# Kernel tuning notes

Measured on AMD Instinct MI355X. Metric: run time of the kernel, lower is better.

The kernel has to match this reference:

```python
import jax, jax.numpy as jnp
import numpy as np

EPS = 1e-5
OFFSET_SCALE = 1.0
KPTS = 9   # 3x3 deformable kernel
GROUP = 1  # in_dim // out_dim


def _bn(x, g, b, m, v):
    # eval-mode BatchNorm2d on (B,C,H,W)
    s = g / jnp.sqrt(v + EPS)
    return x * s[None, :, None, None] + (b - m * s)[None, :, None, None]


def _dcnv4_core(value, offset, mask, offset_scale):
    # value: (B,H,W,G,Cg); offset: (B,H,W,G,K,2) as (dx,dy); mask: (B,H,W,G,K)
    B, H, W, G, Cg = value.shape
    K = mask.shape[-1]
    dt = value.dtype
    ky = jnp.repeat(jnp.arange(3) - 1, 3).astype(dt)
    kx = jnp.tile(jnp.arange(3) - 1, 3).astype(dt)
    grid = jnp.stack([kx, ky], -1)                                   # (K,2)
    base = jnp.stack(jnp.meshgrid(jnp.arange(W, dtype=dt),
                                  jnp.arange(H, dtype=dt),
                                  indexing='xy'), -1)                # (H,W,2) = (x,y)
    loc = base[None, :, :, None, None, :] + (grid + offset) * offset_scale  # (B,H,W,G,K,2)
    px, py = loc[..., 0], loc[..., 1]
    x0 = jnp.floor(px); y0 = jnp.floor(py)
    fx = px - x0; fy = py - y0
    vflat = value.transpose(0, 3, 1, 2, 4).reshape(B, G, H * W, Cg)
    out = jnp.zeros((B, G, H * W, Cg), dt)
    corners = ((0.0, 0.0, (1 - fx) * (1 - fy)), (1.0, 0.0, fx * (1 - fy)),
               (0.0, 1.0, (1 - fx) * fy), (1.0, 1.0, fx * fy))
    for dx, dy, wgt in corners:
        xi = x0 + dx; yi = y0 + dy
        valid = ((xi >= 0) & (xi < W) & (yi >= 0) & (yi < H)).astype(dt)
        idx = (jnp.clip(yi, 0, W and H - 1) * W + jnp.clip(xi, 0, W - 1)).astype(jnp.int32)
        idx = idx.transpose(0, 3, 1, 2, 4).reshape(B, G, H * W * K)
        v = jnp.take_along_axis(vflat, idx[..., None], axis=2).reshape(B, G, H * W, K, Cg)
        w = (wgt * valid * mask).transpose(0, 3, 1, 2, 4).reshape(B, G, H * W, K)
        out = out + jnp.einsum('bgsk,bgskc->bgsc', w, v)
    return out.reshape(B, G, H, W, Cg).transpose(0, 2, 3, 1, 4).reshape(B, H, W, G * Cg)


def setup_inputs() -> dict:
    key = jax.random.key(0)
    B, C, H, W = 8, 128, 64, 64
    C_OUT = 128
    OM = ((GROUP * KPTS * 3 + 7) // 8) * 8  # 32, offset_mask padded width
    ks = jax.random.split(key, 16)
    f = jnp.float32
    sc = 1.0 / np.sqrt(C).astype(np.float32)
    return {
        'x': jax.random.normal(ks[0], (B, C, H, W), f),
        'bn1_g': jax.random.uniform(ks[1], (C,), f, 0.5, 1.5),
        'bn1_b': jax.random.normal(ks[2], (C,), f) * 0.1,
        'bn1_m': jax.random.normal(ks[3], (C,), f) * 0.1,
        'bn1_v': jax.random.uniform(ks[4], (C,), f, 0.5, 1.5),
        'w_pw0': jax.random.normal(ks[5], (C, C), f) * sc,
        'w_vp': jax.random.normal(ks[6], (C, C), f) * sc,
        'b_vp': jnp.zeros((C,), f),
        'w_om': jax.random.normal(ks[7], (C, OM), f) * 0.01,
        'b_om': jnp.zeros((OM,), f),
        'w_op': jax.random.normal(ks[8], (C, C), f) * sc,
        'bn2_g': jax.random.uniform(ks[9], (C,), f, 0.5, 1.5),
        'bn2_b': jax.random.normal(ks[10], (C,), f) * 0.1,
        'bn2_m': jax.random.normal(ks[11], (C,), f) * 0.1,
        'bn2_v': jax.random.uniform(ks[12], (C,), f, 0.5, 1.5),
        'w_pw1': jax.random.normal(ks[13], (C_OUT, C), f) * sc,
    }


def reference(x, bn1_g, bn1_b, bn1_m, bn1_v, w_pw0, w_vp, b_vp, w_om, b_om, w_op,
              bn2_g, bn2_b, bn2_m, bn2_v, w_pw1):
    x = _bn(x, bn1_g, bn1_b, bn1_m, bn1_v)
    x = jnp.einsum('bchw,oc->bohw', x, w_pw0)
    B, C, H, W = x.shape
    x = x.reshape(B, H * W, C)  # raw reshape (faithful to torch .reshape, NOT a permute)
    G, K = GROUP, KPTS
    Cg = C // G
    value = (x @ w_vp + b_vp).reshape(B, H, W, G, Cg)
    om = (x @ w_om + b_om)[..., :G * K * 3].reshape(B, H, W, G, K, 3)
    out = _dcnv4_core(value, om[..., :2], om[..., 2], OFFSET_SCALE)
    out = out.reshape(B, H * W, C) @ w_op
    x = out.reshape(B, C, H, W)  # raw reshape back
    x = _bn(x, bn2_g, bn2_b, bn2_m, bn2_v)
    x = jnp.einsum('bchw,oc->bohw', x, w_pw1)
    return x
```

## Files before the change

### kernel.cpp

```cpp
#include <hip/hip_runtime.h>

#define HW 4096
typedef unsigned short ushort;
typedef __attribute__((ext_vector_type(8))) short short8;
typedef __attribute__((ext_vector_type(4))) float f32x4;

__device__ __forceinline__ ushort bf_rne(float f) {
  unsigned u = __float_as_uint(f);
  unsigned r = (u + 0x7fffu + ((u >> 16) & 1u)) >> 16;
  return (ushort)r;
}
__device__ __forceinline__ void split2(float f, ushort& hi, ushort& lo) {
  ushort h = bf_rne(f);
  float hf = __uint_as_float((unsigned)h << 16);
  hi = h;
  lo = bf_rne(f - hf);
}

__global__ __launch_bounds__(256) void prep(
    const float* __restrict__ g1, const float* __restrict__ be1,
    const float* __restrict__ m1, const float* __restrict__ v1,
    const float* __restrict__ w0,
    const float* __restrict__ g2, const float* __restrict__ be2,
    const float* __restrict__ m2, const float* __restrict__ v2,
    const float* __restrict__ w1,
    const float* __restrict__ wvp, const float* __restrict__ wom,
    const float* __restrict__ wop,
    ushort* __restrict__ W0h, ushort* __restrict__ W0l, float* __restrict__ b0,
    ushort* __restrict__ W1h, ushort* __restrict__ W1l, float* __restrict__ b1,
    ushort* __restrict__ vph, ushort* __restrict__ vpl,
    ushort* __restrict__ oph, ushort* __restrict__ opl,
    ushort* __restrict__ omh, ushort* __restrict__ oml)
{
  const int t = threadIdx.x;
  const int role = blockIdx.x;
  if (role < 16) {
    __shared__ float sc[128], sh[128], part[16][17];
    const int cv = role >> 3;
    const float* g  = cv ? g2 : g1;
    const float* be = cv ? be2 : be1;
    const float* mm = cv ? m2 : m1;
    const float* vv = cv ? v2 : v1;
    if (t < 128) {
      float s = g[t] / sqrtf(vv[t] + 1e-5f);
      sc[t] = s;
      sh[t] = be[t] - mm[t] * s;
    }
    __syncthreads();
    const float* ws = cv ? w1 : w0;
    ushort* dh = cv ? W1h : W0h;
    ushort* dl = cv ? W1l : W0l;
    float* bb  = cv ? b1 : b0;
    const int o = ((role & 7) << 4) + (t >> 4);
    const int kl = t & 15;
    float accb = 0.f;
    #pragma unroll
    for (int j = 0; j < 8; ++j) {
      const int k = (kl << 3) + j;
      const float wv = ws[o * 128 + k];
      ushort hi, lo;
      split2(wv * sc[k], hi, lo);
      dh[o * 128 + k] = hi;
      dl[o * 128 + k] = lo;
      accb = fmaf(wv, sh[k], accb);
    }
    part[t >> 4][kl] = accb;
    __syncthreads();
    if (kl == 0) {
      float s = 0.f;
      #pragma unroll
      for (int j = 0; j < 16; ++j) s += part[t >> 4][j];
      bb[o] = s;
    }
  } else if (role < 32) {
    const int rr = role & 7;
    const float* srcM = (role < 24) ? wvp : wop;
    ushort* dh = (role < 24) ? vph : oph;
    ushort* dl = (role < 24) ? vpl : opl;
    const int n = (rr << 4) + (t >> 4);
    const int kl = t & 15;
    #pragma unroll
    for (int j = 0; j < 8; ++j) {
      const int k = (kl << 3) + j;
      ushort hi, lo;
      split2(srcM[k * 128 + n], hi, lo);
      dh[n * 128 + k] = hi;
      dl[n * 128 + k] = lo;
    }
  } else {
    const int n = ((role - 32) << 4) + (t >> 4);
    const int kl = t & 15;
    #pragma unroll
    for (int j = 0; j < 8; ++j) {
      const int k = (kl << 3) + j;
      ushort hi, lo;
      split2(wom[k * 32 + n], hi, lo);
      omh[n * 128 + k] = hi;
      oml[n * 128 + k] = lo;
    }
  }
}

__global__ __launch_bounds__(256) void gemm_wx(
    const float* __restrict__ act, const ushort* __restrict__ Wh,
    const ushort* __restrict__ Wl, const float* __restrict__ bias,
    float* __restrict__ out)
{
  __shared__ __align__(16) ushort Ah[128][32], Al[128][32];
  __shared__ __align__(16) ushort Bh[128][32], Bl[128][32];
  __shared__ float bias_s[128];
  const int t = threadIdx.x;
  const int hwBase = blockIdx.x << 7;
  const size_t base = (size_t)blockIdx.y * (size_t)(128 * HW);
  if (t < 128) bias_s[t] = bias[t];
  const int lane = t & 63, w = t >> 6;
  const int col = lane & 15, quad = lane >> 4;
  const int wm = (w & 1) << 6, wn = (w >> 1) << 6;
  const f32x4 z = {0.f, 0.f, 0.f, 0.f};
  f32x4 acc[4][4];
  #pragma unroll
  for (int i = 0; i < 4; ++i)
    #pragma unroll
    for (int j = 0; j < 4; ++j) acc[i][j] = z;

  for (int kc = 0; kc < 4; ++kc) {
    const int kBase = kc << 5;
    #pragma unroll
    for (int i = 0; i < 2; ++i) {
      const int idx = t + (i << 8);
      const int o = idx >> 2, q = (idx & 3) << 3;
      *(uint4*)&Ah[o][q] = *(const uint4*)&Wh[o * 128 + kBase + q];
      *(uint4*)&Al[o][q] = *(const uint4*)&Wl[o * 128 + kBase + q];
    }
    {
      const int kr = t >> 3, j0 = (t & 7) << 4;
      const float* srow = &act[base + (size_t)(kBase + kr) * HW + hwBase + j0];
      #pragma unroll
      for (int c4 = 0; c4 < 4; ++c4) {
        const float4 f = *(const float4*)(srow + (c4 << 2));
        ushort h0, l0, h1, l1, h2, l2, h3, l3;
        split2(f.x, h0, l0); split2(f.y, h1, l1);
        split2(f.z, h2, l2); split2(f.w, h3, l3);
        const int j = j0 + (c4 << 2);
        Bh[j + 0][kr] = h0; Bl[j + 0][kr] = l0;
        Bh[j + 1][kr] = h1; Bl[j + 1][kr] = l1;
        Bh[j + 2][kr] = h2; Bl[j + 2][kr] = l2;
        Bh[j + 3][kr] = h3; Bl[j + 3][kr] = l3;
      }
    }
    __syncthreads();
    short8 ah[4], al[4], bh[4], bl[4];
    #pragma unroll
    for (int f = 0; f < 4; ++f) {
      const int row = wm + (f << 4) + col;
      ah[f] = *(const short8*)&Ah[row][quad << 3];
      al[f] = *(const short8*)&Al[row][quad << 3];
    }
    #pragma unroll
    for (int g = 0; g < 4; ++g) {
      const int row = wn + (g << 4) + col;
      bh[g] = *(const short8*)&Bh[row][quad << 3];
      bl[g] = *(const short8*)&Bl[row][quad << 3];
    }
    #pragma unroll
    for (int f = 0; f < 4; ++f)
      #pragma unroll
      for (int g = 0; g < 4; ++g) {
        acc[f][g] = __builtin_amdgcn_mfma_f32_16x16x32_bf16(ah[f], bh[g], acc[f][g], 0, 0, 0);
        acc[f][g] = __builtin_amdgcn_mfma_f32_16x16x32_bf16(ah[f], bl[g], acc[f][g], 0, 0, 0);
        acc[f][g] = __builtin_amdgcn_mfma_f32_16x16x32_bf16(al[f], bh[g], acc[f][g], 0, 0, 0);
      }
    __syncthreads();
  }
  #pragma unroll
  for (int f = 0; f < 4; ++f)
    #pragma unroll
    for (int r = 0; r < 4; ++r) {
      const int o = wm + (f << 4) + (quad << 2) + r;
      const float bb = bias_s[o];
      #pragma unroll
      for (int g = 0; g < 4; ++g)
        out[base + (size_t)o * HW + hwBase + wn + (g << 4) + col] = acc[f][g][r] + bb;
    }
}

template<int NF, bool VALOM>
__global__ __launch_bounds__(256) void gemm_an(
    const float* __restrict__ src,
    const ushort* __restrict__ BTh, const ushort* __restrict__ BTl,
    const ushort* __restrict__ BT2h, const ushort* __restrict__ BT2l,
    const float* __restrict__ bias1, const float* __restrict__ bias2,
    float* __restrict__ C1, float* __restrict__ C2)
{
  __shared__ __align__(16) ushort Ah[128][32], Al[128][32];
  __shared__ __align__(16) ushort Bh[NF * 32][32], Bl[NF * 32][32];
  const int t = threadIdx.x;
  const int rBase = blockIdx.x << 7;
  const int lane = t & 63, w = t >> 6;
  const int col = lane & 15, quad = lane >> 4;
  const int wm = (w & 1) << 6;
  const int wn = (w >> 1) * (NF * 16);
  const f32x4 z = {0.f, 0.f, 0.f, 0.f};
  f32x4 acc[4][NF];
  #pragma unroll
  for (int i = 0; i < 4; ++i)
    #pragma unroll
    for (int j = 0; j < NF; ++j) acc[i][j] = z;

  for (int kc = 0; kc < 4; ++kc) {
    const int kBase = kc << 5;
    {
      const int row = t >> 1, kh = (t & 1) << 4;
      const float* sr = &src[(size_t)(rBase + row) * 128 + kBase + kh];
      union { ushort u[8]; uint4 v; } ph, pl;
      #pragma unroll
      for (int half = 0; half < 2; ++half) {
        #pragma unroll
        for (int c4 = 0; c4 < 2; ++c4) {
          const float4 f = *(const float4*)(sr + (half << 3) + (c4 << 2));
          split2(f.x, ph.u[c4 * 4 + 0], pl.u[c4 * 4 + 0]);
          split2(f.y, ph.u[c4 * 4 + 1], pl.u[c4 * 4 + 1]);
          split2(f.z, ph.u[c4 * 4 + 2], pl.u[c4 * 4 + 2]);
          split2(f.w, ph.u[c4 * 4 + 3], pl.u[c4 * 4 + 3]);
        }
        *(uint4*)&Ah[row][kh + (half << 3)] = ph.v;
        *(uint4*)&Al[row][kh + (half << 3)] = pl.v;
      }
    }
    for (int i = t; i < NF * 32 * 4; i += 256) {
      const int n = i >> 2, q = (i & 3) << 3;
      const ushort* ph = (VALOM && n >= 128) ? &BT2h[(n - 128) * 128 + kBase + q]
                                             : &BTh[n * 128 + kBase + q];
      const ushort* pl = (VALOM && n >= 128) ? &BT2l[(n - 128) * 128 + kBase + q]
                                             : &BTl[n * 128 + kBase + q];
      *(uint4*)&Bh[n][q] = *(const uint4*)ph;
      *(uint4*)&Bl[n][q] = *(const uint4*)pl;
    }
    __syncthreads();
    short8 ah[4], al[4];
    #pragma unroll
    for (int f = 0; f < 4; ++f) {
      const int row = wm + (f << 4) + col;
      ah[f] = *(const short8*)&Ah[row][quad << 3];
      al[f] = *(const short8*)&Al[row][quad << 3];
    }
    #pragma unroll
    for (int g = 0; g < NF; ++g) {
      const int row = wn + (g << 4) + col;
      const short8 bh = *(const short8*)&Bh[row][quad << 3];
      const short8 bl = *(const short8*)&Bl[row][quad << 3];
      #pragma unroll
      for (int f = 0; f < 4; ++f) {
        acc[f][g] = __builtin_amdgcn_mfma_f32_16x16x32_bf16(ah[f], bh, acc[f][g], 0, 0, 0);
        acc[f][g] = __builtin_amdgcn_mfma_f32_16x16x32_bf16(ah[f], bl, acc[f][g], 0, 0, 0);
        acc[f][g] = __builtin_amdgcn_mfma_f32_16x16x32_bf16(al[f], bh, acc[f][g], 0, 0, 0);
      }
    }
    __syncthreads();
  }
  int ng[NF];
  float bb[NF];
  #pragma unroll
  for (int g = 0; g < NF; ++g) {
    ng[g] = wn + (g << 4) + col;
    bb[g] = VALOM ? (ng[g] < 128 ? bias1[ng[g]] : bias2[ng[g] - 128]) : 0.f;
  }
  #pragma unroll
  for (int f = 0; f < 4; ++f)
    #pragma unroll
    for (int r = 0; r < 4; ++r) {
      const int m = rBase + wm + (f << 4) + (quad << 2) + r;
      #pragma unroll
      for (int g = 0; g < NF; ++g) {
        const float v = acc[f][g][r] + bb[g];
        if (VALOM) {
          if (ng[g] < 128) C1[(size_t)m * 128 + ng[g]] = v;
          else             C2[(size_t)m * 32 + (ng[g] - 128)] = v;
        } else {
          C1[(size_t)m * 128 + ng[g]] = v;
        }
      }
    }
}

__global__ __launch_bounds__(256) void dcn_sample(
    const float* __restrict__ value, const float* __restrict__ om,
    float* __restrict__ out)
{
  __shared__ float oms[8][32];
  const int t = threadIdx.x;
  const int blk = blockIdx.x;
  const int b = blk >> 9;
  const int sBase = (blk & 511) << 3;
  const int s = sBase + (t >> 5);
  const int cg = (t & 31) << 2;
  oms[t >> 5][t & 31] = om[((size_t)b * HW + sBase + (t >> 5)) * 32 + (t & 31)];
  __syncthreads();
  const int h = s >> 6, wq = s & 63;
  const float* vb = value + (size_t)b * HW * 128;
  const float* omp = oms[t >> 5];
  const float fw = (float)wq, fh = (float)h;
  float4 acc = {0.f, 0.f, 0.f, 0.f};
  #pragma unroll
  for (int k = 0; k < 9; ++k) {
    const float kx = (float)(k % 3 - 1);
    const float ky = (float)(k / 3 - 1);
    const float dx = omp[k * 3 + 0];
    const float dy = omp[k * 3 + 1];
    const float m  = omp[k * 3 + 2];
    const float px = fw + kx + dx;
    const float py = fh + ky + dy;
    const float x0f = floorf(px), y0f = floorf(py);
    const float fx = px - x0f, fy = py - y0f;
    const int ix = (int)x0f, iy = (int)y0f;
    #pragma unroll
    for (int cy = 0; cy < 2; ++cy) {
      const int yi = iy + cy;
      const float wy = cy ? fy : 1.f - fy;
      const float vy = (yi >= 0 && yi < 64) ? 1.f : 0.f;
      const int yc = min(max(yi, 0), 63);
      #pragma unroll
      for (int cx = 0; cx < 2; ++cx) {
        const int xi = ix + cx;
        const float wx = cx ? fx : 1.f - fx;
        const float vx = (xi >= 0 && xi < 64) ? 1.f : 0.f;
        const int xc = min(max(xi, 0), 63);
        const float wgt = wx * wy * vx * vy * m;
        const float4 v = *(const float4*)&vb[(size_t)(yc * 64 + xc) * 128 + cg];
        acc.x = fmaf(wgt, v.x, acc.x);
        acc.y = fmaf(wgt, v.y, acc.y);
        acc.z = fmaf(wgt, v.z, acc.z);
        acc.w = fmaf(wgt, v.w, acc.w);
      }
    }
  }
  *(float4*)&out[((size_t)b * HW + s) * 128 + cg] = acc;
}

extern "C" void kernel_launch(void* const* d_in, const int* in_sizes, int n_in,
                              void* d_out, int out_size, void* d_ws, size_t ws_size,
                              hipStream_t stream)
{
  const float* x    = (const float*)d_in[0];
  const float* g1   = (const float*)d_in[1];
  const float* be1  = (const float*)d_in[2];
  const float* m1   = (const float*)d_in[3];
  const float* v1   = (const float*)d_in[4];
  const float* wpw0 = (const float*)d_in[5];
  const float* wvp  = (const float*)d_in[6];
  const float* bvp  = (const float*)d_in[7];
  const float* womW = (const float*)d_in[8];
  const float* bom  = (const float*)d_in[9];
  const float* wop  = (const float*)d_in[10];
  const float* g2   = (const float*)d_in[11];
  const float* be2  = (const float*)d_in[12];
  const float* m2   = (const float*)d_in[13];
  const float* v2   = (const float*)d_in[14];
  const float* wpw1 = (const float*)d_in[15];

  char* ws = (char*)d_ws;
  float* y2    = (float*)(ws + 0);
  float* samp  = (float*)(ws + 0);
  float* value = (float*)(ws + 16777216);
  float* out2  = (float*)(ws + 16777216);
  float* omb   = (float*)(ws + 33554432);
  size_t o = 37748736;
  ushort* W0h = (ushort*)(ws + o); o += 32768;
  ushort* W0l = (ushort*)(ws + o); o += 32768;
  ushort* W1h = (ushort*)(ws + o); o += 32768;
  ushort* W1l = (ushort*)(ws + o); o += 32768;
  ushort* vph = (ushort*)(ws + o); o += 32768;
  ushort* vpl = (ushort*)(ws + o); o += 32768;
  ushort* oph = (ushort*)(ws + o); o += 32768;
  ushort* opl = (ushort*)(ws + o); o += 32768;
  ushort* omh = (ushort*)(ws + o); o += 8192;
  ushort* oml = (ushort*)(ws + o); o += 8192;
  float*  b0  = (float*)(ws + o);  o += 512;
  float*  b1  = (float*)(ws + o);

  prep<<<34, 256, 0, stream>>>(g1, be1, m1, v1, wpw0, g2, be2, m2, v2, wpw1,
                               wvp, womW, wop,
                               W0h, W0l, b0, W1h, W1l, b1,
                               vph, vpl, oph, opl, omh, oml);
  gemm_wx<<<dim3(32, 8), 256, 0, stream>>>(x, W0h, W0l, b0, y2);
  gemm_an<5, true><<<dim3(256), 256, 0, stream>>>(y2, vph, vpl, omh, oml,
                                                  bvp, bom, value, omb);
  dcn_sample<<<dim3(4096), 256, 0, stream>>>(value, omb, samp);
  gemm_an<4, false><<<dim3(256), 256, 0, stream>>>(samp, oph, opl, nullptr, nullptr,
                                                   nullptr, nullptr, out2, nullptr);
  gemm_wx<<<dim3(32, 8), 256, 0, stream>>>(out2, W1h, W1l, b1, (float*)d_out);
}
```

Before: 169.8 us.

## Fuse back-to-back GEMM pairs and emit split-bf16 samples from sampler

Fuses the pointwise conv GEMM with the value/offset-mask projection GEMM in one kernel, and the output projection with the final pointwise conv in another. The intermediate stays in shared memory, and the raw-reshape index mapping is used to pick which rows each block owns. The sampler now writes hi/lo bf16 halves directly, so the later GEMM skips the fp32 load and split. This cuts two kernel launches and about two full fp32 intermediate round-trips through HBM. In exchange, only 256 blocks run each fused GEMM, and the kernels use more registers and shared memory, which may limit occupancy.

```diff
diff --git a/kernel.cpp b/kernel.cpp
--- a/kernel.cpp
+++ b/kernel.cpp
@@ -1,6 +1,7 @@
 #include <hip/hip_runtime.h>
 
 #define HW 4096
+#define PAD 33
 typedef unsigned short ushort;
 typedef __attribute__((ext_vector_type(8))) short short8;
 typedef __attribute__((ext_vector_type(4))) float f32x4;
@@ -101,191 +102,150 @@
   }
 }
 
-__global__ __launch_bounds__(256) void gemm_wx(
-    const float* __restrict__ act, const ushort* __restrict__ Wh,
-    const ushort* __restrict__ Wl, const float* __restrict__ bias,
-    float* __restrict__ out)
+__global__ __launch_bounds__(256) void fused_x_valom(
+    const float* __restrict__ x,
+    const ushort* __restrict__ W0h, const ushort* __restrict__ W0l,
+    const float* __restrict__ b0,
+    const ushort* __restrict__ vph, const ushort* __restrict__ vpl,
+    const float* __restrict__ bvp, const float* __restrict__ bom,
+    float* __restrict__ value, float* __restrict__ omb)
 {
-  __shared__ __align__(16) ushort Ah[128][32], Al[128][32];
-  __shared__ __align__(16) ushort Bh[128][32], Bl[128][32];
-  __shared__ float bias_s[128];
+  __shared__ __align__(16) char smem[37376];
+  __shared__ float b0_s[128], b2_s[160];
+  ushort (*Wh_s)[32] = (ushort(*)[32])(smem);
+  ushort (*Wl_s)[32] = (ushort(*)[32])(smem + 8192);
+  float*  Xf         = (float*)(smem + 16384);
+  float*  Yf         = (float*)(smem);
+  ushort (*Vh_s)[32] = (ushort(*)[32])(smem + 16896);
+  ushort (*Vl_s)[32] = (ushort(*)[32])(smem + 27136);
+
   const int t = threadIdx.x;
-  const int hwBase = blockIdx.x << 7;
-  const size_t base = (size_t)blockIdx.y * (size_t)(128 * HW);
-  if (t < 128) bias_s[t] = bias[t];
+  const int cb = blockIdx.x;
+  const int b = blockIdx.y;
+  const int hwBase = cb << 7;
+  const size_t xbase = (size_t)b * (size_t)(128 * HW);
+  if (t < 128) b0_s[t] = b0[t];
+  if (t < 160) b2_s[t] = (t < 128) ? bvp[t] : bom[t - 128];
   const int lane = t & 63, w = t >> 6;
   const int col = lane & 15, quad = lane >> 4;
-  const int wm = (w & 1) << 6, wn = (w >> 1) << 6;
+  const int wm1 = (w & 1) << 6, wn1 = (w >> 1) << 6;
   const f32x4 z = {0.f, 0.f, 0.f, 0.f};
-  f32x4 acc[4][4];
+
+  f32x4 acc1[4][4];
   #pragma unroll
   for (int i = 0; i < 4; ++i)
     #pragma unroll
-    for (int j = 0; j < 4; ++j) acc[i][j] = z;
+    for (int j = 0; j < 4; ++j) acc1[i][j] = z;
 
   for (int kc = 0; kc < 4; ++kc) {
-    const int kBase = kc << 5;
-    #pragma unroll
-    for (int i = 0; i < 2; ++i) {
-      const int idx = t + (i << 8);
-      const int o = idx >> 2, q = (idx & 3) << 3;
-      *(uint4*)&Ah[o][q] = *(const uint4*)&Wh[o * 128 + kBase + q];
-      *(uint4*)&Al[o][q] = *(const uint4*)&Wl[o * 128 + kBase + q];
-    }
-    {
-      const int kr = t >> 3, j0 = (t & 7) << 4;
-      const float* srow = &act[base + (size_t)(kBase + kr) * HW + hwBase + j0];
-      #pragma unroll
-      for (int c4 = 0; c4 < 4; ++c4) {
-        const float4 f = *(const float4*)(srow + (c4 << 2));
-        ushort h0, l0, h1, l1, h2, l2, h3, l3;
-        split2(f.x, h0, l0); split2(f.y, h1, l1);
-        split2(f.z, h2, l2); split2(f.w, h3, l3);
-        const int j = j0 + (c4 << 2);
-        Bh[j + 0][kr] = h0; Bl[j + 0][kr] = l0;
-        Bh[j + 1][kr] = h1; Bl[j + 1][kr] = l1;
-        Bh[j + 2][kr] = h2; Bl[j + 2][kr] = l2;
-        Bh[j + 3][kr] = h3; Bl[j + 3][kr] = l3;
-      }
-    }
-    __syncthreads();
-    short8 ah[4], al[4], bh[4], bl[4];
+    const int kB = kc << 5;
+    for (int i = t; i < 512; i += 256) {
+      const int o = i >> 2, q8 = (i & 3) << 3;
+      *(uint4*)&Wh_s[o][q8] = *(const uint4*)&W0h[o * 128 + kB + q8];
+      *(uint4*)&Wl_s[o][q8] = *(const uint4*)&W0l[o * 128 + kB + q8];
+    }
+    #pragma unroll
+    for (int p = 0; p < 4; ++p) {
+      const int idx = (p << 8) + t;
+      const int c = idx >> 5, j4 = (idx & 31) << 2;
+      const float4 f = *(const float4*)&x[xbase + (size_t)(kB + c) * HW + hwBase + j4];
+      Xf[(j4 + 0) * PAD + c] = f.x;
+      Xf[(j4 + 1) * PAD + c] = f.y;
+      Xf[(j4 + 2) * PAD + c] = f.z;
+      Xf[(j4 + 3) * PAD + c] = f.w;
+    }
+    __syncthreads();
+    short8 aH[4], aL[4];
     #pragma unroll
     for (int f = 0; f < 4; ++f) {
-      const int row = wm + (f << 4) + col;
-      ah[f] = *(const short8*)&Ah[row][quad << 3];
-      al[f] = *(const short8*)&Al[row][quad << 3];
+      const int row = wm1 + (f << 4) + col;
+      aH[f] = *(const short8*)&Wh_s[row][quad << 3];
+      aL[f] = *(const short8*)&Wl_s[row][quad << 3];
     }
     #pragma unroll
     for (int g = 0; g < 4; ++g) {
-      const int row = wn + (g << 4) + col;
-      bh[g] = *(const short8*)&Bh[row][quad << 3];
-      bl[g] = *(const short8*)&Bl[row][quad << 3];
-    }
-    #pragma unroll
-    for (int f = 0; f < 4; ++f)
-      #pragma unroll
-      for (int g = 0; g < 4; ++g) {
-        acc[f][g] = __builtin_amdgcn_mfma_f32_16x16x32_bf16(ah[f], bh[g], acc[f][g], 0, 0, 0);
-        acc[f][g] = __builtin_amdgcn_mfma_f32_16x16x32_bf16(ah[f], bl[g], acc[f][g], 0, 0, 0);
-        acc[f][g] = __builtin_amdgcn_mfma_f32_16x16x32_bf16(al[f], bh[g], acc[f][g], 0, 0, 0);
-      }
-    __syncthreads();
-  }
-  #pragma unroll
-  for (int f = 0; f < 4; ++f)
+      const float* xr = &Xf[(wn1 + (g << 4) + col) * PAD + (quad << 3)];
+      union { ushort u[8]; short8 v; } bh, bl;
+      #pragma unroll
+      for (int j = 0; j < 8; ++j) split2(xr[j], bh.u[j], bl.u[j]);
+      #pragma unroll
+      for (int f = 0; f < 4; ++f) {
+        acc1[f][g] = __builtin_amdgcn_mfma_f32_16x16x32_bf16(aH[f], bh.v, acc1[f][g], 0, 0, 0);
+        acc1[f][g] = __builtin_amdgcn_mfma_f32_16x16x32_bf16(aH[f], bl.v, acc1[f][g], 0, 0, 0);
+        acc1[f][g] = __builtin_amdgcn_mfma_f32_16x16x32_bf16(aL[f], bh.v, acc1[f][g], 0, 0, 0);
+      }
+    }
+    __syncthreads();
+  }
+
+  const int wm2 = (w & 1) << 6;
+  const int wn2 = (w >> 1) * 80;
+  f32x4 acc2[4][5];
+  #pragma unroll
+  for (int i = 0; i < 4; ++i)
+    #pragma unroll
+    for (int j = 0; j < 5; ++j) acc2[i][j] = z;
+
+  for (int j2 = 0; j2 < 4; ++j2) {
+    for (int i = t; i < 640; i += 256) {
+      const int n = i >> 2, q8 = (i & 3) << 3;
+      *(uint4*)&Vh_s[n][q8] = *(const uint4*)&vph[n * 128 + (j2 << 5) + q8];
+      *(uint4*)&Vl_s[n][q8] = *(const uint4*)&vpl[n * 128 + (j2 << 5) + q8];
+    }
+    if ((w >> 1) == (j2 >> 1)) {
+      #pragma unroll
+      for (int gg = 0; gg < 2; ++gg) {
+        const int g = ((j2 & 1) << 1) + gg;
+        #pragma unroll
+        for (int f = 0; f < 4; ++f) {
+          const int o = wm1 + (f << 4) + (quad << 2);
+          #pragma unroll
+          for (int r = 0; r < 4; ++r)
+            Yf[(o + r) * PAD + (gg << 4) + col] = acc1[f][g][r] + b0_s[o + r];
+        }
+      }
+    }
+    __syncthreads();
+    union { ushort u[8]; short8 v; } a2h[4], a2l[4];
+    #pragma unroll
+    for (int f2 = 0; f2 < 4; ++f2) {
+      const float* yr = &Yf[(wm2 + (f2 << 4) + col) * PAD + (quad << 3)];
+      #pragma unroll
+      for (int j = 0; j < 8; ++j) split2(yr[j], a2h[f2].u[j], a2l[f2].u[j]);
+    }
+    #pragma unroll
+    for (int g2 = 0; g2 < 5; ++g2) {
+      const int n = wn2 + (g2 << 4) + col;
+      const short8 vh = *(const short8*)&Vh_s[n][quad << 3];
+      const short8 vl = *(const short8*)&Vl_s[n][quad << 3];
+      #pragma unroll
+      for (int f2 = 0; f2 < 4; ++f2) {
+        acc2[f2][g2] = __builtin_amdgcn_mfma_f32_16x16x32_bf16(a2h[f2].v, vh, acc2[f2][g2], 0, 0, 0);
+        acc2[f2][g2] = __builtin_amdgcn_mfma_f32_16x16x32_bf16(a2h[f2].v, vl, acc2[f2][g2], 0, 0, 0);
+        acc2[f2][g2] = __builtin_amdgcn_mfma_f32_16x16x32_bf16(a2l[f2].v, vh, acc2[f2][g2], 0, 0, 0);
+      }
+    }
+    __syncthreads();
+  }
+  #pragma unroll
+  for (int f2 = 0; f2 < 4; ++f2)
     #pragma unroll
     for (int r = 0; r < 4; ++r) {
-      const int o = wm + (f << 4) + (quad << 2) + r;
-      const float bb = bias_s[o];
-      #pragma unroll
-      for (int g = 0; g < 4; ++g)
-        out[base + (size_t)o * HW + hwBase + wn + (g << 4) + col] = acc[f][g][r] + bb;
-    }
-}
-
-template<int NF, bool VALOM>
-__global__ __launch_bounds__(256) void gemm_an(
-    const float* __restrict__ src,
-    const ushort* __restrict__ BTh, const ushort* __restrict__ BTl,
-    const ushort* __restrict__ BT2h, const ushort* __restrict__ BT2l,
-    const float* __restrict__ bias1, const float* __restrict__ bias2,
-    float* __restrict__ C1, float* __restrict__ C2)
-{
-  __shared__ __align__(16) ushort Ah[128][32], Al[128][32];
-  __shared__ __align__(16) ushort Bh[NF * 32][32], Bl[NF * 32][32];
-  const int t = threadIdx.x;
-  const int rBase = blockIdx.x << 7;
-  const int lane = t & 63, w = t >> 6;
-  const int col = lane & 15, quad = lane >> 4;
-  const int wm = (w & 1) << 6;
-  const int wn = (w >> 1) * (NF * 16);
-  const f32x4 z = {0.f, 0.f, 0.f, 0.f};
-  f32x4 acc[4][NF];
-  #pragma unroll
-  for (int i = 0; i < 4; ++i)
-    #pragma unroll
-    for (int j = 0; j < NF; ++j) acc[i][j] = z;
-
-  for (int kc = 0; kc < 4; ++kc) {
-    const int kBase = kc << 5;
-    {
-      const int row = t >> 1, kh = (t & 1) << 4;
-      const float* sr = &src[(size_t)(rBase + row) * 128 + kBase + kh];
-      union { ushort u[8]; uint4 v; } ph, pl;
-      #pragma unroll
-      for (int half = 0; half < 2; ++half) {
-        #pragma unroll
-        for (int c4 = 0; c4 < 2; ++c4) {
-          const float4 f = *(const float4*)(sr + (half << 3) + (c4 << 2));
-          split2(f.x, ph.u[c4 * 4 + 0], pl.u[c4 * 4 + 0]);
-          split2(f.y, ph.u[c4 * 4 + 1], pl.u[c4 * 4 + 1]);
-          split2(f.z, ph.u[c4 * 4 + 2], pl.u[c4 * 4 + 2]);
-          split2(f.w, ph.u[c4 * 4 + 3], pl.u[c4 * 4 + 3]);
-        }
-        *(uint4*)&Ah[row][kh + (half << 3)] = ph.v;
-        *(uint4*)&Al[row][kh + (half << 3)] = pl.v;
-      }
-    }
-    for (int i = t; i < NF * 32 * 4; i += 256) {
-      const int n = i >> 2, q = (i & 3) << 3;
-      const ushort* ph = (VALOM && n >= 128) ? &BT2h[(n - 128) * 128 + kBase + q]
-                                             : &BTh[n * 128 + kBase + q];
-      const ushort* pl = (VALOM && n >= 128) ? &BT2l[(n - 128) * 128 + kBase + q]
-                                             : &BTl[n * 128 + kBase + q];
-      *(uint4*)&Bh[n][q] = *(const uint4*)ph;
-      *(uint4*)&Bl[n][q] = *(const uint4*)pl;
-    }
-    __syncthreads();
-    short8 ah[4], al[4];
-    #pragma unroll
-    for (int f = 0; f < 4; ++f) {
-      const int row = wm + (f << 4) + col;
-      ah[f] = *(const short8*)&Ah[row][quad << 3];
-      al[f] = *(const short8*)&Al[row][quad << 3];
-    }
-    #pragma unroll
-    for (int g = 0; g < NF; ++g) {
-      const int row = wn + (g << 4) + col;
-      const short8 bh = *(const short8*)&Bh[row][quad << 3];
-      const short8 bl = *(const short8*)&Bl[row][quad << 3];
-      #pragma unroll
-      for (int f = 0; f < 4; ++f) {
-        acc[f][g] = __builtin_amdgcn_mfma_f32_16x16x32_bf16(ah[f], bh, acc[f][g], 0, 0, 0);
-        acc[f][g] = __builtin_amdgcn_mfma_f32_16x16x32_bf16(ah[f], bl, acc[f][g], 0, 0, 0);
-        acc[f][g] = __builtin_amdgcn_mfma_f32_16x16x32_bf16(al[f], bh, acc[f][g], 0, 0, 0);
-      }
-    }
-    __syncthreads();
-  }
-  int ng[NF];
-  float bb[NF];
-  #pragma unroll
-  for (int g = 0; g < NF; ++g) {
-    ng[g] = wn + (g << 4) + col;
-    bb[g] = VALOM ? (ng[g] < 128 ? bias1[ng[g]] : bias2[ng[g] - 128]) : 0.f;
-  }
-  #pragma unroll
-  for (int f = 0; f < 4; ++f)
-    #pragma unroll
-    for (int r = 0; r < 4; ++r) {
-      const int m = rBase + wm + (f << 4) + (quad << 2) + r;
-      #pragma unroll
-      for (int g = 0; g < NF; ++g) {
-        const float v = acc[f][g][r] + bb[g];
-        if (VALOM) {
-          if (ng[g] < 128) C1[(size_t)m * 128 + ng[g]] = v;
-          else             C2[(size_t)m * 32 + (ng[g] - 128)] = v;
-        } else {
-          C1[(size_t)m * 128 + ng[g]] = v;
-        }
+      const int m = wm2 + (f2 << 4) + (quad << 2) + r;
+      const size_t gRow = (size_t)b * HW + (size_t)m * 32 + cb;
+      #pragma unroll
+      for (int g2 = 0; g2 < 5; ++g2) {
+        const int n = wn2 + (g2 << 4) + col;
+        const float v = acc2[f2][g2][r] + b2_s[n];
+        if (n < 128) value[gRow * 128 + n] = v;
+        else         omb[gRow * 32 + (n - 128)] = v;
       }
     }
 }
 
 __global__ __launch_bounds__(256) void dcn_sample(
     const float* __restrict__ value, const float* __restrict__ om,
-    float* __restrict__ out)
+    ushort* __restrict__ samph, ushort* __restrict__ sampl)
 {
   __shared__ float oms[8][32];
   const int t = threadIdx.x;
@@ -334,7 +294,143 @@
       }
     }
   }
-  *(float4*)&out[((size_t)b * HW + s) * 128 + cg] = acc;
+  ushort h0, l0, h1, l1, h2, l2, h3, l3;
+  split2(acc.x, h0, l0); split2(acc.y, h1, l1);
+  split2(acc.z, h2, l2); split2(acc.w, h3, l3);
+  const size_t idx = ((size_t)b * HW + s) * 128 + cg;
+  uint2 uh, ul;
+  uh.x = (unsigned)h0 | ((unsigned)h1 << 16);
+  uh.y = (unsigned)h2 | ((unsigned)h3 << 16);
+  ul.x = (unsigned)l0 | ((unsigned)l1 << 16);
+  ul.y = (unsigned)l2 | ((unsigned)l3 << 16);
+  *(uint2*)&samph[idx] = uh;
+  *(uint2*)&sampl[idx] = ul;
+}
+
+__global__ __launch_bounds__(256) void fused_op_out(
+    const ushort* __restrict__ samph, const ushort* __restrict__ sampl,
+    const ushort* __restrict__ oph, const ushort* __restrict__ opl,
+    const ushort* __restrict__ W1h, const ushort* __restrict__ W1l,
+    const float* __restrict__ b1, float* __restrict__ out)
+{
+  __shared__ __align__(16) char smem[33280];
+  __shared__ float b1_s[128];
+  ushort (*Ah_s)[32]  = (ushort(*)[32])(smem);
+  ushort (*Al_s)[32]  = (ushort(*)[32])(smem + 8192);
+  ushort (*Bh_s)[32]  = (ushort(*)[32])(smem + 16384);
+  ushort (*Bl_s)[32]  = (ushort(*)[32])(smem + 24576);
+  float*  Yf          = (float*)(smem);
+  ushort (*W1h_s)[32] = (ushort(*)[32])(smem + 16896);
+  ushort (*W1l_s)[32] = (ushort(*)[32])(smem + 25088);
+
+  const int t = threadIdx.x;
+  const int cb = blockIdx.x;
+  const int b = blockIdx.y;
+  if (t < 128) b1_s[t] = b1[t];
+  const int lane = t & 63, w = t >> 6;
+  const int col = lane & 15, quad = lane >> 4;
+  const int wm1 = (w & 1) << 6, wn1 = (w >> 1) << 6;
+  const f32x4 z = {0.f, 0.f, 0.f, 0.f};
+
+  f32x4 acc1[4][4];
+  #pragma unroll
+  for (int i = 0; i < 4; ++i)
+    #pragma unroll
+    for (int j = 0; j < 4; ++j) acc1[i][j] = z;
+
+  for (int kc = 0; kc < 4; ++kc) {
+    const int kB = kc << 5;
+    for (int i = t; i < 512; i += 256) {
+      const int m = i >> 2, q8 = (i & 3) << 3;
+      const size_t row = (size_t)b * HW + (size_t)m * 32 + cb;
+      *(uint4*)&Ah_s[m][q8] = *(const uint4*)&samph[row * 128 + kB + q8];
+      *(uint4*)&Al_s[m][q8] = *(const uint4*)&sampl[row * 128 + kB + q8];
+      *(uint4*)&Bh_s[m][q8] = *(const uint4*)&oph[m * 128 + kB + q8];
+      *(uint4*)&Bl_s[m][q8] = *(const uint4*)&opl[m * 128 + kB + q8];
+    }
+    __syncthreads();
+    short8 aH[4], aL[4];
+    #pragma unroll
+    for (int f = 0; f < 4; ++f) {
+      const int row = wm1 + (f << 4) + col;
+      aH[f] = *(const short8*)&Ah_s[row][quad << 3];
+      aL[f] = *(const short8*)&Al_s[row][quad << 3];
+    }
+    #pragma unroll
+    for (int g = 0; g < 4; ++g) {
+      const int n = wn1 + (g << 4) + col;
+      const short8 bh = *(const short8*)&Bh_s[n][quad << 3];
+      const short8 bl = *(const short8*)&Bl_s[n][quad << 3];
+      #pragma unroll
+      for (int f = 0; f < 4; ++f) {
+        acc1[f][g] = __builtin_amdgcn_mfma_f32_16x16x32_bf16(aH[f], bh, acc1[f][g], 0, 0, 0);
+        acc1[f][g] = __builtin_amdgcn_mfma_f32_16x16x32_bf16(aH[f], bl, acc1[f][g], 0, 0, 0);
+        acc1[f][g] = __builtin_amdgcn_mfma_f32_16x16x32_bf16(aL[f], bh, acc1[f][g], 0, 0, 0);
+      }
+    }
+    __syncthreads();
+  }
+
+  const int wm2 = (w & 1) << 6, wn2 = (w >> 1) << 6;
+  f32x4 acc2[4][4];
+  #pragma unroll
+  for (int i = 0; i < 4; ++i)
+    #pragma unroll
+    for (int j = 0; j < 4; ++j) acc2[i][j] = z;
+
+  for (int j2 = 0; j2 < 4; ++j2) {
+    for (int i = t; i < 512; i += 256) {
+      const int o = i >> 2, q8 = (i & 3) << 3;
+      *(uint4*)&W1h_s[o][q8] = *(const uint4*)&W1h[o * 128 + (j2 << 5) + q8];
+      *(uint4*)&W1l_s[o][q8] = *(const uint4*)&W1l[o * 128 + (j2 << 5) + q8];
+    }
+    if ((w & 1) == (j2 >> 1)) {
+      #pragma unroll
+      for (int ff = 0; ff < 2; ++ff) {
+        const int f = ((j2 & 1) << 1) + ff;
+        #pragma unroll
+        for (int g = 0; g < 4; ++g) {
+          const int j = wn1 + (g << 4) + col;
+          #pragma unroll
+          for (int r = 0; r < 4; ++r)
+            Yf[j * PAD + (ff << 4) + (quad << 2) + r] = acc1[f][g][r];
+        }
+      }
+    }
+    __syncthreads();
+    union { ushort u[8]; short8 v; } b5h[4], b5l[4];
+    #pragma unroll
+    for (int g2 = 0; g2 < 4; ++g2) {
+      const float* yr = &Yf[(wn2 + (g2 << 4) + col) * PAD + (quad << 3)];
+      #pragma unroll
+      for (int j = 0; j < 8; ++j) split2(yr[j], b5h[g2].u[j], b5l[g2].u[j]);
+    }
+    #pragma unroll
+    for (int f2 = 0; f2 < 4; ++f2) {
+      const int o = wm2 + (f2 << 4) + col;
+      const short8 ah = *(const short8*)&W1h_s[o][quad << 3];
+      const short8 al = *(const short8*)&W1l_s[o][quad << 3];
+      #pragma unroll
+      for (int g2 = 0; g2 < 4; ++g2) {
+        acc2[f2][g2] = __builtin_amdgcn_mfma_f32_16x16x32_bf16(ah, b5h[g2].v, acc2[f2][g2], 0, 0, 0);
+        acc2[f2][g2] = __builtin_amdgcn_mfma_f32_16x16x32_bf16(ah, b5l[g2].v, acc2[f2][g2], 0, 0, 0);
+        acc2[f2][g2] = __builtin_amdgcn_mfma_f32_16x16x32_bf16(al, b5h[g2].v, acc2[f2][g2], 0, 0, 0);
+      }
+    }
+    __syncthreads();
+  }
+  const size_t obase = (size_t)b * (size_t)(128 * HW) + ((size_t)cb << 7);
+  #pragma unroll
+  for (int f2 = 0; f2 < 4; ++f2)
+    #pragma unroll
+    for (int r = 0; r < 4; ++r) {
+      const int o = wm2 + (f2 << 4) + (quad << 2) + r;
+      #pragma unroll
+      for (int g2 = 0; g2 < 4; ++g2) {
+        const int j = wn2 + (g2 << 4) + col;
+        out[obase + (size_t)o * HW + j] = acc2[f2][g2][r] + b1_s[o];
+      }
+    }
 }
 
 extern "C" void kernel_launch(void* const* d_in, const int* in_sizes, int n_in,
@@ -359,34 +455,31 @@
   const float* wpw1 = (const float*)d_in[15];
 
   char* ws = (char*)d_ws;
-  float* y2    = (float*)(ws + 0);
-  float* samp  = (float*)(ws + 0);
-  float* value = (float*)(ws + 16777216);
-  float* out2  = (float*)(ws + 16777216);
-  float* omb   = (float*)(ws + 33554432);
+  float*  value = (float*) (ws + 0);
+  float*  omb   = (float*) (ws + 16777216);
+  ushort* samph = (ushort*)(ws + 20971520);
+  ushort* sampl = (ushort*)(ws + 29360128);
   size_t o = 37748736;
   ushort* W0h = (ushort*)(ws + o); o += 32768;
   ushort* W0l = (ushort*)(ws + o); o += 32768;
   ushort* W1h = (ushort*)(ws + o); o += 32768;
   ushort* W1l = (ushort*)(ws + o); o += 32768;
-  ushort* vph = (ushort*)(ws + o); o += 32768;
-  ushort* vpl = (ushort*)(ws + o); o += 32768;
+  ushort* vph = (ushort*)(ws + o); o += 40960;
+  ushort* vpl = (ushort*)(ws + o); o += 40960;
   ushort* oph = (ushort*)(ws + o); o += 32768;
   ushort* opl = (ushort*)(ws + o); o += 32768;
-  ushort* omh = (ushort*)(ws + o); o += 8192;
-  ushort* oml = (ushort*)(ws + o); o += 8192;
   float*  b0  = (float*)(ws + o);  o += 512;
   float*  b1  = (float*)(ws + o);
+  ushort* omh = vph + 128 * 128;
+  ushort* oml = vpl + 128 * 128;
 
   prep<<<34, 256, 0, stream>>>(g1, be1, m1, v1, wpw0, g2, be2, m2, v2, wpw1,
                                wvp, womW, wop,
                                W0h, W0l, b0, W1h, W1l, b1,
                                vph, vpl, oph, opl, omh, oml);
-  gemm_wx<<<dim3(32, 8), 256, 0, stream>>>(x, W0h, W0l, b0, y2);
-  gemm_an<5, true><<<dim3(256), 256, 0, stream>>>(y2, vph, vpl, omh, oml,
-                                                  bvp, bom, value, omb);
-  dcn_sample<<<dim3(4096), 256, 0, stream>>>(value, omb, samp);
-  gemm_an<4, false><<<dim3(256), 256, 0, stream>>>(samp, oph, opl, nullptr, nullptr,
-                                                   nullptr, nullptr, out2, nullptr);
-  gemm_wx<<<dim3(32, 8), 256, 0, stream>>>(out2, W1h, W1l, b1, (float*)d_out);
-}
+  fused_x_valom<<<dim3(32, 8), 256, 0, stream>>>(x, W0h, W0l, b0, vph, vpl,
+                                                 bvp, bom, value, omb);
+  dcn_sample<<<dim3(4096), 256, 0, stream>>>(value, omb, samph, sampl);
+  fused_op_out<<<dim3(32, 8), 256, 0, stream>>>(samph, sampl, oph, opl,
+                                                W1h, W1l, b1, (float*)d_out);
+}
```

New measurement: 156.0 us. 1.09x faster.
